# Kernel optimization log

Measured on AMD Instinct MI355X. Metric: run time of the kernel, lower is better.

## Reference

```python
import jax, jax.numpy as jnp
import numpy as np

B = 4096          # batch_size per view
D = 256           # projection feature dim
TEMP_F = 0.5      # temperature_f


def setup_inputs() -> dict:
    key = jax.random.key(0)
    k1, k2 = jax.random.split(key)
    return {
        "h_i": jax.random.normal(k1, (B, D), dtype=jnp.float32),
        "h_j": jax.random.normal(k2, (B, D), dtype=jnp.float32),
    }


def reference(h_i, h_j):
    # NT-Xent contrastive loss (forward_feature).
    batch = h_i.shape[0]
    N = 2 * batch
    h = jnp.concatenate([h_i, h_j], axis=0)                 # [N, D]
    sim = (h @ h.T) / TEMP_F                                # [N, N]

    # positives: sim(i, i+batch) and sim(i+batch, i)
    sim_i_j = jnp.diagonal(sim, offset=batch)               # [batch]
    sim_j_i = jnp.diagonal(sim, offset=-batch)              # [batch]
    pos = jnp.concatenate([sim_i_j, sim_j_i], axis=0)       # [N]

    # Torch builds logits = [pos_i, negatives_i] per row where negatives are
    # sim[i, :] with the diagonal AND the positive-pair entry removed, then
    # takes CE with label 0. Since the removed positive-pair entry equals
    # pos_i itself, logsumexp(logits_i) == logsumexp(sim[i, :] with only the
    # diagonal masked). So: loss_i = logsumexp(sim_masked[i]) - pos_i.
    neg_inf = jnp.finfo(sim.dtype).min
    eye = jnp.eye(N, dtype=bool)
    sim_masked = jnp.where(eye, neg_inf, sim)               # mask self-similarity
    lse = jax.nn.logsumexp(sim_masked, axis=1)              # [N]

    # CrossEntropyLoss(reduction='sum') / N  == mean over rows
    loss = jnp.mean(lse - pos)
    return loss
```

## Files before the change

kernel.cpp:

```cpp
#include <hip/hip_runtime.h>
#include <hip/hip_bf16.h>
#include <stdint.h>

#define BATCH 4096
#define N_TOT 8192
#define D_DIM 256
#define SHIFT 150.0f
#define SQRT2 1.41421356237309515f

typedef __bf16 bf16_t;
typedef bf16_t bf16x8 __attribute__((ext_vector_type(8)));
typedef bf16_t bf16x4 __attribute__((ext_vector_type(4)));
typedef float f32x4 __attribute__((ext_vector_type(4)));

__device__ __forceinline__ void gl_lds16(const void* g, void* l) {
  __builtin_amdgcn_global_load_lds(
      (const __attribute__((address_space(1))) void*)(uintptr_t)g,
      (__attribute__((address_space(3))) void*)(uint32_t)(uintptr_t)l,
      16, 0, 0);
}

__global__ void k_prep(const float* __restrict__ hi, const float* __restrict__ hj,
                       bf16_t* __restrict__ hb, float* __restrict__ Zrow,
                       float* __restrict__ posPartial) {
  const int wave = threadIdx.x >> 6, lane = threadIdx.x & 63;
  const int r = blockIdx.x * 4 + wave;
  const size_t off = (size_t)r * D_DIM + lane * 4;
  float4 a = *(const float4*)(hi + off);
  float4 b = *(const float4*)(hj + off);

  bf16x4 oa, ob;
  oa[0] = (bf16_t)(a.x * SQRT2); oa[1] = (bf16_t)(a.y * SQRT2);
  oa[2] = (bf16_t)(a.z * SQRT2); oa[3] = (bf16_t)(a.w * SQRT2);
  ob[0] = (bf16_t)(b.x * SQRT2); ob[1] = (bf16_t)(b.y * SQRT2);
  ob[2] = (bf16_t)(b.z * SQRT2); ob[3] = (bf16_t)(b.w * SQRT2);
  *(bf16x4*)(hb + off) = oa;
  *(bf16x4*)(hb + (size_t)BATCH * D_DIM + off) = ob;

  float d = a.x * b.x + a.y * b.y + a.z * b.z + a.w * b.w;
#pragma unroll
  for (int o = 32; o >= 1; o >>= 1) d += __shfl_xor(d, o);
  __shared__ float ps[4];
  if (lane == 0) ps[wave] = d;
  if (threadIdx.x < 8) Zrow[blockIdx.x * 8 + threadIdx.x] = 0.f;
  __syncthreads();
  if (threadIdx.x == 0) posPartial[blockIdx.x] = ps[0] + ps[1] + ps[2] + ps[3];
}

__global__ __launch_bounds__(256, 4) void k_gemm(const bf16_t* __restrict__ hb,
                                                 float* __restrict__ Zrow) {
  const int t = blockIdx.x;
  int bj = (int)((sqrtf(8.0f * (float)t + 1.0f) - 1.0f) * 0.5f);
  while ((bj + 1) * (bj + 2) / 2 <= t) ++bj;
  while (bj * (bj + 1) / 2 > t) --bj;
  const int bi = t - bj * (bj + 1) / 2;
  const int rBase = bi * 128;
  const int cBase = bj * 128;
  const bool diag = (bi == bj);

  __shared__ __align__(16) bf16_t As[128][64];
  __shared__ __align__(16) bf16_t Bs[128][64];
  const int tid = threadIdx.x;
  const int lane = tid & 63;
  const int wave = tid >> 6;

  const int half = wave & 1;
  const size_t stageRow = (size_t)((wave < 2 ? rBase : cBase) + half * 64);
  const int c_src = (lane & 7) ^ (lane >> 3);
  const bf16_t* gsrc = hb + stageRow * D_DIM + (size_t)(lane >> 3) * D_DIM + c_src * 8;
  bf16_t* lbase = (wave < 2) ? &As[half * 64][0] : &Bs[half * 64][0];

  const int wm = wave >> 1, wn = wave & 1;
  const int quad = lane >> 4, l16 = lane & 15;
  const int sw = l16 & 7;

  f32x4 acc[4][4];
#pragma unroll
  for (int i = 0; i < 4; ++i)
#pragma unroll
    for (int j = 0; j < 4; ++j) acc[i][j] = (f32x4){0.f, 0.f, 0.f, 0.f};

#pragma unroll
  for (int kc = 0; kc < 4; ++kc) {
    __syncthreads();
#pragma unroll
    for (int i = 0; i < 8; ++i)
      gl_lds16(gsrc + (size_t)i * 8 * D_DIM + kc * 64, lbase + i * 8 * 64);
    __syncthreads();
#pragma unroll
    for (int ks = 0; ks < 2; ++ks) {
      bf16x8 af[4], bfr[4];
      const int chunk = ((ks * 4 + quad) ^ sw) * 8;
#pragma unroll
      for (int mt = 0; mt < 4; ++mt)
        af[mt] = *(const bf16x8*)&As[wm * 64 + mt * 16 + l16][chunk];
#pragma unroll
      for (int nt = 0; nt < 4; ++nt)
        bfr[nt] = *(const bf16x8*)&Bs[wn * 64 + nt * 16 + l16][chunk];
#pragma unroll
      for (int mt = 0; mt < 4; ++mt)
#pragma unroll
        for (int nt = 0; nt < 4; ++nt)
          acc[mt][nt] = __builtin_amdgcn_mfma_f32_16x16x32_bf16(af[mt], bfr[nt],
                                                                acc[mt][nt], 0, 0, 0);
    }
  }

  const int rW = rBase + wm * 64 + quad * 4;
  const int cW = cBase + wn * 64 + l16;
  float colAcc[4] = {0.f, 0.f, 0.f, 0.f};
#pragma unroll
  for (int mt = 0; mt < 4; ++mt) {
#pragma unroll
    for (int rg = 0; rg < 4; ++rg) {
      const int rr = rW + mt * 16 + rg;
      float s = 0.f;
#pragma unroll
      for (int nt = 0; nt < 4; ++nt) {
        float e = __expf(acc[mt][nt][rg] - SHIFT);
        if (diag && (rr == cW + nt * 16)) e = 0.f;
        s += e;
        colAcc[nt] += e;
      }
      s += __shfl_xor(s, 1);
      s += __shfl_xor(s, 2);
      s += __shfl_xor(s, 4);
      s += __shfl_xor(s, 8);
      if (l16 == 0) atomicAdd(&Zrow[rr], s);
    }
  }
  if (!diag) {
#pragma unroll
    for (int nt = 0; nt < 4; ++nt) {
      float c = colAcc[nt];
      c += __shfl_xor(c, 16);
      c += __shfl_xor(c, 32);
      if (lane < 16) atomicAdd(&Zrow[cW + nt * 16], c);
    }
  }
}

__global__ void k_finish(const float* __restrict__ Zrow,
                         const float* __restrict__ posPartial,
                         float* __restrict__ out) {
  const int t = threadIdx.x;
  float4 z0 = *(const float4*)(Zrow + t * 8);
  float4 z1 = *(const float4*)(Zrow + t * 8 + 4);
  float sl = __logf(z0.x) + __logf(z0.y) + __logf(z0.z) + __logf(z0.w) +
             __logf(z1.x) + __logf(z1.y) + __logf(z1.z) + __logf(z1.w);
  float sp = posPartial[t];
#pragma unroll
  for (int o = 32; o >= 1; o >>= 1) {
    sl += __shfl_xor(sl, o);
    sp += __shfl_xor(sp, o);
  }
  __shared__ float pl[16], pp[16];
  const int wave = t >> 6, lane = t & 63;
  if (lane == 0) { pl[wave] = sl; pp[wave] = sp; }
  __syncthreads();
  if (t == 0) {
    float L = 0.f, P = 0.f;
    for (int i = 0; i < 16; ++i) { L += pl[i]; P += pp[i]; }
    out[0] = L / (float)N_TOT + SHIFT - P / 2048.0f;
  }
}

extern "C" void kernel_launch(void* const* d_in, const int* in_sizes, int n_in,
                              void* d_out, int out_size, void* d_ws, size_t ws_size,
                              hipStream_t stream) {
  const float* hi = (const float*)d_in[0];
  const float* hj = (const float*)d_in[1];
  float* out = (float*)d_out;

  bf16_t* hb = (bf16_t*)d_ws;
  float* Zrow = (float*)((char*)d_ws + (size_t)N_TOT * D_DIM * 2);
  float* posPartial = Zrow + N_TOT;

  k_prep<<<1024, 256, 0, stream>>>(hi, hj, hb, Zrow, posPartial);
  k_gemm<<<2080, 256, 0, stream>>>(hb, Zrow);
  k_finish<<<1, 1024, 0, stream>>>(Zrow, posPartial, out);
}
```

Baseline: 95.67 us.

## Load GEMM fragments directly from global memory, dropping LDS staging

The GEMM kernel no longer stages A/B tiles through shared memory with async global-to-LDS loads. Each wave now reads its MFMA operand fragments straight from global memory (relying on L1/L2 caching), which removes both __syncthreads per k-chunk. The occupancy hint in launch bounds drops from 4 to 2 blocks per CU, giving the compiler more registers for the larger set of in-flight loads. The cost is that data shared between waves is fetched repeatedly rather than once, and the loads are narrow and strided across rows.

```diff
diff --git a/kernel.cpp b/kernel.cpp
--- a/kernel.cpp
+++ b/kernel.cpp
@@ -12,13 +12,6 @@
 typedef bf16_t bf16x8 __attribute__((ext_vector_type(8)));
 typedef bf16_t bf16x4 __attribute__((ext_vector_type(4)));
 typedef float f32x4 __attribute__((ext_vector_type(4)));
-
-__device__ __forceinline__ void gl_lds16(const void* g, void* l) {
-  __builtin_amdgcn_global_load_lds(
-      (const __attribute__((address_space(1))) void*)(uintptr_t)g,
-      (__attribute__((address_space(3))) void*)(uint32_t)(uintptr_t)l,
-      16, 0, 0);
-}
 
 __global__ void k_prep(const float* __restrict__ hi, const float* __restrict__ hj,
                        bf16_t* __restrict__ hb, float* __restrict__ Zrow,
@@ -47,7 +40,7 @@
   if (threadIdx.x == 0) posPartial[blockIdx.x] = ps[0] + ps[1] + ps[2] + ps[3];
 }
 
-__global__ __launch_bounds__(256, 4) void k_gemm(const bf16_t* __restrict__ hb,
+__global__ __launch_bounds__(256, 2) void k_gemm(const bf16_t* __restrict__ hb,
                                                  float* __restrict__ Zrow) {
   const int t = blockIdx.x;
   int bj = (int)((sqrtf(8.0f * (float)t + 1.0f) - 1.0f) * 0.5f);
@@ -58,21 +51,13 @@
   const int cBase = bj * 128;
   const bool diag = (bi == bj);
 
-  __shared__ __align__(16) bf16_t As[128][64];
-  __shared__ __align__(16) bf16_t Bs[128][64];
-  const int tid = threadIdx.x;
-  const int lane = tid & 63;
-  const int wave = tid >> 6;
-
-  const int half = wave & 1;
-  const size_t stageRow = (size_t)((wave < 2 ? rBase : cBase) + half * 64);
-  const int c_src = (lane & 7) ^ (lane >> 3);
-  const bf16_t* gsrc = hb + stageRow * D_DIM + (size_t)(lane >> 3) * D_DIM + c_src * 8;
-  bf16_t* lbase = (wave < 2) ? &As[half * 64][0] : &Bs[half * 64][0];
-
+  const int lane = threadIdx.x & 63;
+  const int wave = threadIdx.x >> 6;
   const int wm = wave >> 1, wn = wave & 1;
   const int quad = lane >> 4, l16 = lane & 15;
-  const int sw = l16 & 7;
+
+  const bf16_t* aptr = hb + (size_t)(rBase + wm * 64 + l16) * D_DIM + quad * 8;
+  const bf16_t* bptr = hb + (size_t)(cBase + wn * 64 + l16) * D_DIM + quad * 8;
 
   f32x4 acc[4][4];
 #pragma unroll
@@ -81,29 +66,20 @@
     for (int j = 0; j < 4; ++j) acc[i][j] = (f32x4){0.f, 0.f, 0.f, 0.f};
 
 #pragma unroll
-  for (int kc = 0; kc < 4; ++kc) {
-    __syncthreads();
+  for (int ks = 0; ks < 8; ++ks) {
+    bf16x8 af[4], bfr[4];
 #pragma unroll
-    for (int i = 0; i < 8; ++i)
-      gl_lds16(gsrc + (size_t)i * 8 * D_DIM + kc * 64, lbase + i * 8 * 64);
-    __syncthreads();
+    for (int mt = 0; mt < 4; ++mt)
+      af[mt] = *(const bf16x8*)(aptr + (size_t)mt * 16 * D_DIM + ks * 32);
 #pragma unroll
-    for (int ks = 0; ks < 2; ++ks) {
-      bf16x8 af[4], bfr[4];
-      const int chunk = ((ks * 4 + quad) ^ sw) * 8;
+    for (int nt = 0; nt < 4; ++nt)
+      bfr[nt] = *(const bf16x8*)(bptr + (size_t)nt * 16 * D_DIM + ks * 32);
 #pragma unroll
-      for (int mt = 0; mt < 4; ++mt)
-        af[mt] = *(const bf16x8*)&As[wm * 64 + mt * 16 + l16][chunk];
+    for (int mt = 0; mt < 4; ++mt)
 #pragma unroll
       for (int nt = 0; nt < 4; ++nt)
-        bfr[nt] = *(const bf16x8*)&Bs[wn * 64 + nt * 16 + l16][chunk];
-#pragma unroll
-      for (int mt = 0; mt < 4; ++mt)
-#pragma unroll
-        for (int nt = 0; nt < 4; ++nt)
-          acc[mt][nt] = __builtin_amdgcn_mfma_f32_16x16x32_bf16(af[mt], bfr[nt],
-                                                                acc[mt][nt], 0, 0, 0);
-    }
+        acc[mt][nt] = __builtin_amdgcn_mfma_f32_16x16x32_bf16(af[mt], bfr[nt],
+                                                              acc[mt][nt], 0, 0, 0);
   }
 
   const int rW = rBase + wm * 64 + quad * 4;
```

New measurement: 134.6 us. +40.7%, slower.
